# Performance work log

Measured on AMD Instinct MI355X. Metric: run time of the kernel, lower is better.

Reference implementation:

```python
import jax, jax.numpy as jnp
import numpy as np

N = 50000          # nodes
E = 800000         # edges (COO, no self loops; added during normalization)
D = 100            # input_dim
H = 16             # gcn_hidden_dim
C = 40             # output_dim (classes)
MAX_HOPS = 3
REPL = 3
NC = REPL * (MAX_HOPS + 1)   # 12 cells
BN_EPS = 1e-5


def setup_inputs() -> dict:
    key = jax.random.key(0)
    ks = jax.random.split(key, 12)
    x = jax.random.normal(ks[0], (N, D), jnp.float32)
    edge_row = jax.random.randint(ks[1], (E,), 0, N, dtype=jnp.int32)
    edge_col = jax.random.randint(ks[2], (E,), 0, N, dtype=jnp.int32)
    # stacked per-cell parameters, cell index i = r*(MAX_HOPS+1)+h
    W1 = jax.random.normal(ks[3], (NC, D, H), jnp.float32) / np.sqrt(D)
    b1 = jax.random.normal(ks[4], (NC, H), jnp.float32) * 0.01
    gamma = jnp.ones((NC, H), jnp.float32)
    beta = jnp.zeros((NC, H), jnp.float32)
    bn_mean = jnp.zeros((NC, H), jnp.float32)
    bn_var = jnp.ones((NC, H), jnp.float32)
    W2 = jax.random.normal(ks[5], (NC, H, C), jnp.float32) / np.sqrt(H)
    b2 = jax.random.normal(ks[6], (NC, C), jnp.float32) * 0.01
    Wout = jax.random.normal(ks[7], (NC * C, C), jnp.float32) / np.sqrt(NC * C)
    bout = jax.random.normal(ks[8], (C,), jnp.float32) * 0.01
    return {"x": x, "edge_row": edge_row, "edge_col": edge_col,
            "W1": W1, "b1": b1, "gamma": gamma, "beta": beta,
            "bn_mean": bn_mean, "bn_var": bn_var,
            "W2": W2, "b2": b2, "Wout": Wout, "bout": bout}


def _norm_adj(edge_row, edge_col, dtype):
    # GCN symmetric normalization with self loops: D^-1/2 (A+I) D^-1/2
    loops = jnp.arange(N, dtype=edge_row.dtype)
    row = jnp.concatenate([edge_row, loops])
    col = jnp.concatenate([edge_col, loops])
    ones = jnp.ones(row.shape[0], dtype)
    deg = jax.ops.segment_sum(ones, row, num_segments=N)
    dinv = jnp.where(deg > 0, jax.lax.rsqrt(deg), jnp.zeros_like(deg))
    vals = dinv[row] * dinv[col]
    return row, col, vals


def reference(x, edge_row, edge_col, W1, b1, gamma, beta, bn_mean, bn_var,
              W2, b2, Wout, bout):
    row, col, vals = _norm_adj(edge_row, edge_col, x.dtype)

    def spmm(h):  # [N,F] -> [N,F]  out[i] = sum_e vals[e]*h[col[e]] at row[e]
        return jax.ops.segment_sum(vals[:, None] * h[col], row, num_segments=N)

    # eval mode: input dropout = identity; L2-normalize rows
    xn = x / jnp.maximum(jnp.linalg.norm(x, axis=1, keepdims=True), 1e-12)

    # A^h x shared across replicas
    xs = [xn]
    for _ in range(MAX_HOPS):
        xs.append(spmm(xs[-1]))

    outs = []
    for r in range(REPL):
        for h in range(MAX_HOPS + 1):
            i = r * (MAX_HOPS + 1) + h
            hid = xs[h] @ W1[i] + b1[i]
            # BatchNorm1d in eval mode (running stats), then ReLU; dropout = identity
            hid = (hid - bn_mean[i]) * (gamma[i] * jax.lax.rsqrt(bn_var[i] + BN_EPS)) + beta[i]
            hid = jax.nn.relu(hid)
            for _ in range(h):
                hid = spmm(hid)
            outs.append(hid @ W2[i] + b2[i])

    cell_outputs = jnp.stack(outs, axis=1)              # [N, NC, C]
    flat = jax.nn.relu(cell_outputs.reshape(N, NC * C))
    output = flat @ Wout + bout                          # [N, C]
    return (output, cell_outputs)
```

## Files before the change

### kernel.cpp

```cpp
#include <hip/hip_runtime.h>
#include <hip/hip_bf16.h>

#define NN 50000
#define EE 800000
#define DD 100
#define HH 16
#define CC 40
#define NCELL 12
#define NB_SCAN 49

typedef __hip_bfloat162 bf2;
typedef short bf16x8 __attribute__((ext_vector_type(8)));
typedef float f32x4 __attribute__((ext_vector_type(4)));

__device__ __forceinline__ float2 b2f2(bf2 v) { return __bfloat1622float2(v); }
__device__ __forceinline__ bf2 f22b2(float f0, float f1) {
    float2 t; t.x = f0; t.y = f1;
    return __float22bfloat162_rn(t);
}
__device__ __forceinline__ unsigned short f2b(float f) {
    __hip_bfloat16 h = __float2bfloat16(f);
    return *reinterpret_cast<unsigned short*>(&h);
}


__global__ __launch_bounds__(256) void k_hist(const int* __restrict__ er, int* __restrict__ cnt) {
    int e = blockIdx.x * 256 + threadIdx.x;
    if (e < EE) atomicAdd(&cnt[er[e]], 1);
}

__global__ __launch_bounds__(256) void k_dinv(const int* __restrict__ cnt, float* __restrict__ dinv) {
    int i = blockIdx.x * 256 + threadIdx.x;
    if (i < NN) dinv[i] = rsqrtf((float)(cnt[i] + 1));
}

__global__ __launch_bounds__(1024) void k_scan1(const int* __restrict__ cnt, int* __restrict__ rp,
                                                int* __restrict__ bsum) {
    __shared__ int lds[1024];
    int t = threadIdx.x, i = blockIdx.x * 1024 + t;
    int v = (i < NN) ? cnt[i] : 0;
    lds[t] = v;
    __syncthreads();
    #pragma unroll
    for (int off = 1; off < 1024; off <<= 1) {
        int x = lds[t];
        int y = (t >= off) ? lds[t - off] : 0;
        __syncthreads();
        lds[t] = x + y;
        __syncthreads();
    }
    if (i < NN) rp[i] = lds[t] - v;
    if (t == 1023) bsum[blockIdx.x] = lds[1023];
}

__global__ __launch_bounds__(64) void k_scan2(int* __restrict__ bsum) {
    int t = threadIdx.x;
    int orig = (t < NB_SCAN) ? bsum[t] : 0;
    int v = orig;
    #pragma unroll
    for (int off = 1; off < 64; off <<= 1) {
        int y = __shfl_up(v, off);
        if (t >= off) v += y;
    }
    if (t < NB_SCAN) bsum[t] = v - orig;
    if (t == NB_SCAN - 1) bsum[NB_SCAN] = v;
}

__global__ __launch_bounds__(256) void k_scan3(int* __restrict__ rp, int* __restrict__ cursor,
                                               const int* __restrict__ bsum) {
    int i = blockIdx.x * 256 + threadIdx.x;
    if (i < NN) {
        int v = rp[i] + bsum[i >> 10];
        rp[i] = v;
        cursor[i] = v;
    }
    if (i == 0) rp[NN] = bsum[NB_SCAN];
}

__global__ __launch_bounds__(256) void k_fill(const int* __restrict__ er, const int* __restrict__ ec,
                                              const float* __restrict__ dinv, int* __restrict__ cursor,
                                              int* __restrict__ ci, float* __restrict__ cv) {
    int e = blockIdx.x * 256 + threadIdx.x;
    if (e >= EE) return;
    int r = er[e], c = ec[e];
    int p = atomicAdd(&cursor[r], 1);
    ci[p] = c;
    cv[p] = dinv[r] * dinv[c];
}

__global__ __launch_bounds__(256) void k_normx(const float* __restrict__ x, bf2* __restrict__ xb) {
    int wid = (blockIdx.x * 256 + threadIdx.x) >> 6;
    int lane = threadIdx.x & 63;
    if (wid >= NN) return;
    const size_t base = (size_t)wid * DD;
    int c0 = 2 * lane;
    float a = (c0 < DD) ? x[base + c0] : 0.f;
    float b = (c0 + 1 < DD) ? x[base + c0 + 1] : 0.f;
    float ss = a * a + b * b;
    #pragma unroll
    for (int off = 1; off < 64; off <<= 1) ss += __shfl_xor(ss, off);
    float inv = 1.f / fmaxf(sqrtf(ss), 1e-12f);
    xb[(size_t)wid * 64 + lane] = f22b2(a * inv, b * inv);
}

__global__ __launch_bounds__(256) void k_w1t(const float* __restrict__ W1, const float* __restrict__ gamma,
                                             const float* __restrict__ bn_var, unsigned short* __restrict__ W1T) {
    int idx = blockIdx.x * 256 + threadIdx.x;
    if (idx >= 192 * 128) return;
    int c = idx / 128, k = idx % 128;
    int g = c / 48, i = c % 48;
    int cell = (i / 16) * 4 + g, j = i % 16;
    float sc = gamma[cell * HH + j] * rsqrtf(bn_var[cell * HH + j] + 1e-5f);
    float v = (k < DD) ? W1[((size_t)cell * DD + k) * HH + j] * sc : 0.f;
    W1T[idx] = f2b(v);
}

__global__ __launch_bounds__(256) void k_proj_mfma(const bf2* __restrict__ xb,
                                                   const unsigned short* __restrict__ W1T,
                                                   unsigned short* __restrict__ Pu) {
    int tid = threadIdx.x;
    int wid = tid >> 6, lane = tid & 63;
    int rowbase = blockIdx.x * 64 + wid * 16;
    int arow = rowbase + (lane & 15);
    int arow_c = (arow < NN) ? arow : NN - 1;
    int kgrp = lane >> 4;
    int bcol = lane & 15;

    f32x4 acc[12];
    #pragma unroll
    for (int t = 0; t < 12; t++) acc[t] = (f32x4){0.f, 0.f, 0.f, 0.f};

    const unsigned short* ap = (const unsigned short*)(xb + (size_t)arow_c * 64);
    for (int kt = 0; kt < 4; kt++) {
        int k0 = kt * 32 + kgrp * 8;
        bf16x8 afr = *(const bf16x8*)(ap + k0);
        #pragma unroll
        for (int t = 0; t < 12; t++) {
            bf16x8 bfr = *(const bf16x8*)(W1T + (size_t)(t * 16 + bcol) * 128 + k0);
            acc[t] = __builtin_amdgcn_mfma_f32_16x16x32_bf16(afr, bfr, acc[t], 0, 0, 0);
        }
    }
    int drow = rowbase + (lane >> 4) * 4;
    #pragma unroll
    for (int r = 0; r < 4; r++) {
        int grow = drow + r;
        if (grow < NN) {
            unsigned short* pr = Pu + (size_t)grow * 192;
            #pragma unroll
            for (int t = 0; t < 12; t++)
                pr[t * 16 + (lane & 15)] = f2b(acc[t][r]);
        }
    }
}

template <int NU, int RPW>
__global__ __launch_bounds__(256) void k_spmm(const int* __restrict__ rp, const int* __restrict__ ci,
                                              const float* __restrict__ cv, const float* __restrict__ dinv,
                                              const bf2* __restrict__ in, int ins, int ioff,
                                              bf2* __restrict__ out, int outs) {
    constexpr int LPR = (RPW == 1) ? 64 : 32;
    constexpr int J = (NU + LPR - 1) / LPR;
    int gw = (blockIdx.x * 256 + threadIdx.x) >> 6;
    int lane = threadIdx.x & 63;
    int sub = (RPW == 2) ? (lane >> 5) : 0;
    int su = (RPW == 2) ? (lane & 31) : lane;
    int row = gw * RPW + sub;
    if (row >= NN) return;
    const bf2* ib = in + ioff;

    float d = dinv[row];
    float sw = d * d;
    float2 acc[J];
    {
        size_t b = (size_t)row * ins;
        #pragma unroll
        for (int j = 0; j < J; j++) {
            int u = su + LPR * j;
            if (u < NU) {
                float2 f = b2f2(ib[b + u]);
                acc[j].x = sw * f.x; acc[j].y = sw * f.y;
            } else { acc[j].x = 0.f; acc[j].y = 0.f; }
        }
    }
    int s = rp[row], e = rp[row + 1];
    int p = s;
    int e4 = s + ((e - s) & ~3);
    while (p < e4) {
        int c0 = ci[p], c1 = ci[p + 1], c2 = ci[p + 2], c3 = ci[p + 3];
        float v0 = cv[p], v1 = cv[p + 1], v2 = cv[p + 2], v3 = cv[p + 3];
        bf2 r0[J], r1[J], r2[J], r3[J];
        size_t b0 = (size_t)c0 * ins, b1 = (size_t)c1 * ins, b2 = (size_t)c2 * ins, b3 = (size_t)c3 * ins;
        #pragma unroll
        for (int j = 0; j < J; j++) {
            int u = su + LPR * j;
            if (u < NU) {
                r0[j] = ib[b0 + u]; r1[j] = ib[b1 + u];
                r2[j] = ib[b2 + u]; r3[j] = ib[b3 + u];
            }
        }
        #pragma unroll
        for (int j = 0; j < J; j++) {
            int u = su + LPR * j;
            if (u < NU) {
                float2 f0 = b2f2(r0[j]), f1 = b2f2(r1[j]), f2 = b2f2(r2[j]), f3 = b2f2(r3[j]);
                acc[j].x += v0 * f0.x + v1 * f1.x + v2 * f2.x + v3 * f3.x;
                acc[j].y += v0 * f0.y + v1 * f1.y + v2 * f2.y + v3 * f3.y;
            }
        }
        p += 4;
    }
    while (p < e) {
        int c = ci[p];
        float v = cv[p];
        size_t b = (size_t)c * ins;
        #pragma unroll
        for (int j = 0; j < J; j++) {
            int u = su + LPR * j;
            if (u < NU) {
                float2 f = b2f2(ib[b + u]);
                acc[j].x += v * f.x; acc[j].y += v * f.y;
            }
        }
        p++;
    }
    size_t ob = (size_t)row * outs;
    #pragma unroll
    for (int j = 0; j < J; j++) {
        int u = su + LPR * j;
        if (u < NU) out[ob + u] = f22b2(acc[j].x, acc[j].y);
    }
}

__global__ __launch_bounds__(256) void k_bnrelu(const bf2* __restrict__ P, const bf2* __restrict__ R1,
                                                const bf2* __restrict__ R2, const bf2* __restrict__ R3,
                                                const float* __restrict__ b1, const float* __restrict__ gamma,
                                                const float* __restrict__ beta, const float* __restrict__ bn_mean,
                                                const float* __restrict__ bn_var,
                                                bf2* __restrict__ H0, bf2* __restrict__ H123) {
    int idx = blockIdx.x * 256 + threadIdx.x;
    if (idx >= NN * 96) return;
    int n = idx / 96, u = idx % 96;
    int h, su;
    bf2 v;
    if (u < 24) { h = 0; su = u; v = P[(size_t)n * 96 + su]; }
    else {
        int uu = u - 24;
        h = uu / 24 + 1; su = uu % 24;
        if (h == 1)      v = R1[(size_t)n * 72 + su];
        else if (h == 2) v = R2[(size_t)n * 48 + su];
        else             v = R3[(size_t)n * 24 + su];
    }
    int c0 = 2 * su;
    int cell = (c0 / 16) * 4 + h;
    int j0 = c0 % 16;
    int i0 = cell * HH + j0, i1 = i0 + 1;
    float s0 = gamma[i0] * rsqrtf(bn_var[i0] + 1e-5f);
    float s1 = gamma[i1] * rsqrtf(bn_var[i1] + 1e-5f);
    float sh0 = (b1[i0] - bn_mean[i0]) * s0 + beta[i0];
    float sh1 = (b1[i1] - bn_mean[i1]) * s1 + beta[i1];
    float2 f = b2f2(v);
    bf2 o = f22b2(fmaxf(f.x + sh0, 0.f), fmaxf(f.y + sh1, 0.f));
    if (u < 24) H0[(size_t)n * 24 + u] = o;
    else        H123[(size_t)n * 72 + (u - 24)] = o;
}

#define NUNITS 1024
__global__ __launch_bounds__(128) void k_cellout(const bf2* __restrict__ H0, const bf2* __restrict__ U1,
                                                 const bf2* __restrict__ U2, const bf2* __restrict__ U3,
                                                 const float* __restrict__ W2, const float* __restrict__ b2v,
                                                 float* __restrict__ outcell) {
    __shared__ float row[2][200];
    int tid = threadIdx.x;
    int gid = tid;
    bool act = gid < 120;
    int cell = act ? gid / 10 : 0;
    int cc = act ? (4 * gid) % 40 : 0;
    int h = cell & 3, r = cell >> 2;
    float4 wreg[HH];
    float4 bias = make_float4(0.f, 0.f, 0.f, 0.f);
    if (act) {
        #pragma unroll
        for (int k = 0; k < HH; k++)
            wreg[k] = *(const float4*)(W2 + (size_t)cell * (HH * CC) + k * CC + cc);
        bias = *(const float4*)(b2v + cell * CC + cc);
    }
    int colbase = h * 48 + r * 16;

    const bf2* tabs[4] = {H0, U1, U2, U3};
    const int strides[4] = {24, 72, 48, 24};

    int iters = (NN + NUNITS - 1) / NUNITS;
    int n_cur = blockIdx.x;
    if (tid < 96 && n_cur < NN) {
        int t4 = tid / 24, uu = tid % 24;
        float2 f = b2f2(tabs[t4][(size_t)n_cur * strides[t4] + uu]);
        row[0][t4 * 48 + 2 * uu] = f.x;
        row[0][t4 * 48 + 2 * uu + 1] = f.y;
    }
    __syncthreads();
    for (int it = 0; it < iters; it++) {
        int buf = it & 1;
        int n_next = n_cur + NUNITS;
        if (it + 1 < iters && tid < 96 && n_next < NN) {
            int t4 = tid / 24, uu = tid % 24;
            float2 f = b2f2(tabs[t4][(size_t)n_next * strides[t4] + uu]);
            row[buf ^ 1][t4 * 48 + 2 * uu] = f.x;
            row[buf ^ 1][t4 * 48 + 2 * uu + 1] = f.y;
        }
        if (act && n_cur < NN) {
            float4 acc = bias;
            #pragma unroll
            for (int k = 0; k < HH; k++) {
                float xv = row[buf][colbase + k];
                acc.x += xv * wreg[k].x;
                acc.y += xv * wreg[k].y;
                acc.z += xv * wreg[k].z;
                acc.w += xv * wreg[k].w;
            }
            *(float4*)(outcell + (size_t)n_cur * (NCELL * CC) + 4 * gid) = acc;
        }
        __syncthreads();
        n_cur = n_next;
    }
}

__global__ __launch_bounds__(256) void k_wt(const float* __restrict__ Wout, unsigned short* __restrict__ WoutT) {
    int idx = blockIdx.x * 256 + threadIdx.x;
    if (idx >= 48 * 480) return;
    int c = idx / 480, k = idx % 480;
    float v = (c < CC) ? Wout[(size_t)k * CC + c] : 0.f;
    WoutT[idx] = f2b(v);
}

__global__ __launch_bounds__(256) void k_final_mfma(const float* __restrict__ cell,
                                                    const unsigned short* __restrict__ WoutT,
                                                    const float* __restrict__ bout, float* __restrict__ out) {
    int tid = threadIdx.x;
    int wid = tid >> 6, lane = tid & 63;
    int rowbase = blockIdx.x * 64 + wid * 16;
    int arow = rowbase + (lane & 15);
    int arow_c = (arow < NN) ? arow : NN - 1;
    int kgrp = lane >> 4;

    f32x4 acc0 = {0.f, 0.f, 0.f, 0.f};
    f32x4 acc1 = {0.f, 0.f, 0.f, 0.f};
    f32x4 acc2 = {0.f, 0.f, 0.f, 0.f};

    const float* arow_p = cell + (size_t)arow_c * (NCELL * CC);
    int bcol = lane & 15;

    for (int kt = 0; kt < 15; kt++) {
        int k0 = kt * 32 + kgrp * 8;
        float4 va = *(const float4*)(arow_p + k0);
        float4 vb = *(const float4*)(arow_p + k0 + 4);
        bf16x8 afr;
        afr[0] = (short)f2b(fmaxf(va.x, 0.f));
        afr[1] = (short)f2b(fmaxf(va.y, 0.f));
        afr[2] = (short)f2b(fmaxf(va.z, 0.f));
        afr[3] = (short)f2b(fmaxf(va.w, 0.f));
        afr[4] = (short)f2b(fmaxf(vb.x, 0.f));
        afr[5] = (short)f2b(fmaxf(vb.y, 0.f));
        afr[6] = (short)f2b(fmaxf(vb.z, 0.f));
        afr[7] = (short)f2b(fmaxf(vb.w, 0.f));
        bf16x8 bf0 = *(const bf16x8*)(WoutT + (size_t)(0 * 16 + bcol) * 480 + k0);
        bf16x8 bf1 = *(const bf16x8*)(WoutT + (size_t)(1 * 16 + bcol) * 480 + k0);
        bf16x8 bf2f = *(const bf16x8*)(WoutT + (size_t)(2 * 16 + bcol) * 480 + k0);
        acc0 = __builtin_amdgcn_mfma_f32_16x16x32_bf16(afr, bf0, acc0, 0, 0, 0);
        acc1 = __builtin_amdgcn_mfma_f32_16x16x32_bf16(afr, bf1, acc1, 0, 0, 0);
        acc2 = __builtin_amdgcn_mfma_f32_16x16x32_bf16(afr, bf2f, acc2, 0, 0, 0);
    }

    int drow = rowbase + (lane >> 4) * 4;
    #pragma unroll
    for (int r = 0; r < 4; r++) {
        int grow = drow + r;
        if (grow < NN) {
            int c0 = 0 * 16 + (lane & 15);
            int c1 = 1 * 16 + (lane & 15);
            int c2 = 2 * 16 + (lane & 15);
            float* o = out + (size_t)grow * CC;
            o[c0] = acc0[r] + bout[c0];
            o[c1] = acc1[r] + bout[c1];
            if (c2 < CC) o[c2] = acc2[r] + bout[c2];
        }
    }
}


extern "C" void kernel_launch(void* const* d_in, const int* in_sizes, int n_in,
                              void* d_out, int out_size, void* d_ws, size_t ws_size,
                              hipStream_t stream) {
    const float* x       = (const float*)d_in[0];
    const int*   er      = (const int*)d_in[1];
    const int*   ec      = (const int*)d_in[2];
    const float* W1      = (const float*)d_in[3];
    const float* b1      = (const float*)d_in[4];
    const float* gamma   = (const float*)d_in[5];
    const float* beta    = (const float*)d_in[6];
    const float* bn_mean = (const float*)d_in[7];
    const float* bn_var  = (const float*)d_in[8];
    const float* W2      = (const float*)d_in[9];
    const float* b2v     = (const float*)d_in[10];
    const float* Wout    = (const float*)d_in[11];
    const float* bout    = (const float*)d_in[12];

    float* out     = (float*)d_out;
    float* outcell = out + (size_t)NN * CC;

    char* w = (char*)d_ws;
    auto alloc = [&](size_t bytes) {
        void* p = (void*)w;
        w += (bytes + 255) & ~(size_t)255;
        return p;
    };
    int*   cnt    = (int*)alloc((size_t)NN * 4);
    int*   rp     = (int*)alloc((size_t)(NN + 1) * 4);
    int*   cursor = (int*)alloc((size_t)NN * 4);
    float* dinv   = (float*)alloc((size_t)NN * 4);
    int*   bsum   = (int*)alloc((size_t)(NB_SCAN + 1) * 4);
    int*   ci     = (int*)alloc((size_t)EE * 4);
    float* cv     = (float*)alloc((size_t)EE * 4);
    bf2*   xb     = (bf2*)alloc((size_t)NN * 64 * 4);
    bf2*   P      = (bf2*)alloc((size_t)NN * 96 * 4);
    bf2*   R1     = (bf2*)alloc((size_t)NN * 72 * 4);
    bf2*   R2     = (bf2*)alloc((size_t)NN * 48 * 4);
    bf2*   R3     = (bf2*)alloc((size_t)NN * 24 * 4);
    bf2*   H0     = (bf2*)alloc((size_t)NN * 24 * 4);
    bf2*   H123   = (bf2*)alloc((size_t)NN * 72 * 4);
    bf2*   U1     = (bf2*)alloc((size_t)NN * 72 * 4);
    bf2*   U2     = (bf2*)alloc((size_t)NN * 48 * 4);
    bf2*   U3     = (bf2*)alloc((size_t)NN * 24 * 4);
    unsigned short* WoutT = (unsigned short*)alloc((size_t)48 * 480 * 2);
    unsigned short* W1T   = (unsigned short*)alloc((size_t)192 * 128 * 2);

    hipMemsetAsync(cnt, 0, (size_t)NN * 4, stream);

    int gE = (EE + 255) / 256;
    int gN = (NN + 255) / 256;

    k_hist<<<gE, 256, 0, stream>>>(er, cnt);
    k_dinv<<<gN, 256, 0, stream>>>(cnt, dinv);
    k_scan1<<<NB_SCAN, 1024, 0, stream>>>(cnt, rp, bsum);
    k_scan2<<<1, 64, 0, stream>>>(bsum);
    k_scan3<<<gN, 256, 0, stream>>>(rp, cursor, bsum);
    k_fill<<<gE, 256, 0, stream>>>(er, ec, dinv, cursor, ci, cv);
    k_wt<<<(48 * 480 + 255) / 256, 256, 0, stream>>>(Wout, WoutT);
    k_w1t<<<(192 * 128 + 255) / 256, 256, 0, stream>>>(W1, gamma, bn_var, W1T);

    int gW = (NN + 3) / 4;
    int g64 = (NN + 63) / 64;
    k_normx<<<gW, 256, 0, stream>>>(x, xb);
    k_proj_mfma<<<g64, 256, 0, stream>>>(xb, W1T, (unsigned short*)P);

    int gW1 = (NN + 3) / 4;
    int gW2 = (NN + 7) / 8;
    k_spmm<72, 1><<<gW1, 256, 0, stream>>>(rp, ci, cv, dinv, P, 96, 24, R1, 72);
    k_spmm<48, 1><<<gW1, 256, 0, stream>>>(rp, ci, cv, dinv, R1, 72, 24, R2, 48);
    k_spmm<24, 2><<<gW2, 256, 0, stream>>>(rp, ci, cv, dinv, R2, 48, 24, R3, 24);

    k_bnrelu<<<(NN * 96 + 255) / 256, 256, 0, stream>>>(P, R1, R2, R3, b1, gamma, beta, bn_mean, bn_var, H0, H123);

    k_spmm<72, 1><<<gW1, 256, 0, stream>>>(rp, ci, cv, dinv, H123, 72, 0, U1, 72);
    k_spmm<48, 1><<<gW1, 256, 0, stream>>>(rp, ci, cv, dinv, U1, 72, 24, U2, 48);
    k_spmm<24, 2><<<gW2, 256, 0, stream>>>(rp, ci, cv, dinv, U2, 48, 24, U3, 24);

    k_cellout<<<NUNITS, 128, 0, stream>>>(H0, U1, U2, U3, W2, b2v, outcell);
    k_final_mfma<<<g64, 256, 0, stream>>>(outcell, WoutT, bout, out);
}
```

Measured before the change: 457.8 us.

## Fuse BN/ReLU into projection and SpMM epilogues, drop finished columns, MFMA cell output

After: 504.2 us. +10.1%, slower.

```diff
diff --git a/kernel.cpp b/kernel.cpp
--- a/kernel.cpp
+++ b/kernel.cpp
@@ -115,9 +115,35 @@
     W1T[idx] = f2b(v);
 }
 
+__global__ __launch_bounds__(256) void k_shift(const float* __restrict__ b1, const float* __restrict__ gamma,
+                                               const float* __restrict__ beta, const float* __restrict__ bn_mean,
+                                               const float* __restrict__ bn_var, float* __restrict__ shift192) {
+    int c = blockIdx.x * 256 + threadIdx.x;
+    if (c >= 192) return;
+    int h = c / 48, r = (c % 48) / 16, j = c % 16;
+    int i = (r * 4 + h) * HH + j;
+    float sc = gamma[i] * rsqrtf(bn_var[i] + 1e-5f);
+    shift192[c] = (b1[i] - bn_mean[i]) * sc + beta[i];
+}
+
+__global__ __launch_bounds__(256) void k_w2p(const float* __restrict__ W2, unsigned short* __restrict__ Wpack) {
+    int idx = blockIdx.x * 256 + threadIdx.x;
+    if (idx >= 30 * 16 * 32) return;
+    int t = idx / 512, bcol = (idx / 32) % 16, k = idx % 32;
+    int c = 16 * t + bcol;
+    int cell = c / 40, cc = c % 40;
+    int m = (2 * t) / 5; if (m > 10) m = 10;
+    int kg = 16 * m + k;
+    int cellk = kg / 16, j = kg % 16;
+    float v = (cellk == cell) ? W2[((size_t)cell * HH + j) * CC + cc] : 0.f;
+    Wpack[idx] = f2b(v);
+}
+
 __global__ __launch_bounds__(256) void k_proj_mfma(const bf2* __restrict__ xb,
                                                    const unsigned short* __restrict__ W1T,
-                                                   unsigned short* __restrict__ Pu) {
+                                                   const float* __restrict__ shift192,
+                                                   unsigned short* __restrict__ Hcat,
+                                                   unsigned short* __restrict__ Pg) {
     int tid = threadIdx.x;
     int wid = tid >> 6, lane = tid & 63;
     int rowbase = blockIdx.x * 64 + wid * 16;
@@ -141,23 +167,33 @@
         }
     }
     int drow = rowbase + (lane >> 4) * 4;
+    int lc = lane & 15;
     #pragma unroll
     for (int r = 0; r < 4; r++) {
         int grow = drow + r;
         if (grow < NN) {
-            unsigned short* pr = Pu + (size_t)grow * 192;
             #pragma unroll
-            for (int t = 0; t < 12; t++)
-                pr[t * 16 + (lane & 15)] = f2b(acc[t][r]);
-        }
-    }
-}
-
-template <int NU, int RPW>
+            for (int t = 0; t < 12; t++) {
+                int c = t * 16 + lc;
+                float v = acc[t][r];
+                if (c < 48) {
+                    v = fmaxf(v + shift192[c], 0.f);
+                    Hcat[(size_t)grow * 192 + (c / 16) * 64 + (c % 16)] = f2b(v);
+                } else {
+                    Pg[(size_t)grow * 144 + (c - 48)] = f2b(v);
+                }
+            }
+        }
+    }
+}
+
+template <int NU, int RPW, bool RELU, bool HMAP>
 __global__ __launch_bounds__(256) void k_spmm(const int* __restrict__ rp, const int* __restrict__ ci,
                                               const float* __restrict__ cv, const float* __restrict__ dinv,
-                                              const bf2* __restrict__ in, int ins, int ioff,
-                                              bf2* __restrict__ out, int outs) {
+                                              const bf2* __restrict__ in, int ins,
+                                              bf2* __restrict__ outA, int sA, int aoff,
+                                              const float* __restrict__ shiftA,
+                                              bf2* __restrict__ outB, int sB) {
     constexpr int LPR = (RPW == 1) ? 64 : 32;
     constexpr int J = (NU + LPR - 1) / LPR;
     int gw = (blockIdx.x * 256 + threadIdx.x) >> 6;
@@ -166,7 +202,6 @@
     int su = (RPW == 2) ? (lane & 31) : lane;
     int row = gw * RPW + sub;
     if (row >= NN) return;
-    const bf2* ib = in + ioff;
 
     float d = dinv[row];
     float sw = d * d;
@@ -177,37 +212,41 @@
         for (int j = 0; j < J; j++) {
             int u = su + LPR * j;
             if (u < NU) {
-                float2 f = b2f2(ib[b + u]);
+                float2 f = b2f2(in[b + u]);
                 acc[j].x = sw * f.x; acc[j].y = sw * f.y;
             } else { acc[j].x = 0.f; acc[j].y = 0.f; }
         }
     }
     int s = rp[row], e = rp[row + 1];
     int p = s;
-    int e4 = s + ((e - s) & ~3);
-    while (p < e4) {
-        int c0 = ci[p], c1 = ci[p + 1], c2 = ci[p + 2], c3 = ci[p + 3];
-        float v0 = cv[p], v1 = cv[p + 1], v2 = cv[p + 2], v3 = cv[p + 3];
-        bf2 r0[J], r1[J], r2[J], r3[J];
-        size_t b0 = (size_t)c0 * ins, b1 = (size_t)c1 * ins, b2 = (size_t)c2 * ins, b3 = (size_t)c3 * ins;
-        #pragma unroll
-        for (int j = 0; j < J; j++) {
-            int u = su + LPR * j;
-            if (u < NU) {
-                r0[j] = ib[b0 + u]; r1[j] = ib[b1 + u];
-                r2[j] = ib[b2 + u]; r3[j] = ib[b3 + u];
+    int e8 = s + ((e - s) & ~7);
+    while (p < e8) {
+        int cc8[8]; float vv[8];
+        #pragma unroll
+        for (int q = 0; q < 8; q++) { cc8[q] = ci[p + q]; vv[q] = cv[p + q]; }
+        bf2 rr[8][J];
+        #pragma unroll
+        for (int q = 0; q < 8; q++) {
+            size_t b = (size_t)cc8[q] * ins;
+            #pragma unroll
+            for (int j = 0; j < J; j++) {
+                int u = su + LPR * j;
+                if (u < NU) rr[q][j] = in[b + u];
             }
         }
         #pragma unroll
-        for (int j = 0; j < J; j++) {
-            int u = su + LPR * j;
-            if (u < NU) {
-                float2 f0 = b2f2(r0[j]), f1 = b2f2(r1[j]), f2 = b2f2(r2[j]), f3 = b2f2(r3[j]);
-                acc[j].x += v0 * f0.x + v1 * f1.x + v2 * f2.x + v3 * f3.x;
-                acc[j].y += v0 * f0.y + v1 * f1.y + v2 * f2.y + v3 * f3.y;
+        for (int q = 0; q < 8; q++) {
+            #pragma unroll
+            for (int j = 0; j < J; j++) {
+                int u = su + LPR * j;
+                if (u < NU) {
+                    float2 f = b2f2(rr[q][j]);
+                    acc[j].x += vv[q] * f.x;
+                    acc[j].y += vv[q] * f.y;
+                }
             }
         }
-        p += 4;
+        p += 8;
     }
     while (p < e) {
         int c = ci[p];
@@ -217,110 +256,62 @@
         for (int j = 0; j < J; j++) {
             int u = su + LPR * j;
             if (u < NU) {
-                float2 f = b2f2(ib[b + u]);
+                float2 f = b2f2(in[b + u]);
                 acc[j].x += v * f.x; acc[j].y += v * f.y;
             }
         }
         p++;
     }
-    size_t ob = (size_t)row * outs;
     #pragma unroll
     for (int j = 0; j < J; j++) {
         int u = su + LPR * j;
-        if (u < NU) out[ob + u] = f22b2(acc[j].x, acc[j].y);
-    }
-}
-
-__global__ __launch_bounds__(256) void k_bnrelu(const bf2* __restrict__ P, const bf2* __restrict__ R1,
-                                                const bf2* __restrict__ R2, const bf2* __restrict__ R3,
-                                                const float* __restrict__ b1, const float* __restrict__ gamma,
-                                                const float* __restrict__ beta, const float* __restrict__ bn_mean,
-                                                const float* __restrict__ bn_var,
-                                                bf2* __restrict__ H0, bf2* __restrict__ H123) {
-    int idx = blockIdx.x * 256 + threadIdx.x;
-    if (idx >= NN * 96) return;
-    int n = idx / 96, u = idx % 96;
-    int h, su;
-    bf2 v;
-    if (u < 24) { h = 0; su = u; v = P[(size_t)n * 96 + su]; }
-    else {
-        int uu = u - 24;
-        h = uu / 24 + 1; su = uu % 24;
-        if (h == 1)      v = R1[(size_t)n * 72 + su];
-        else if (h == 2) v = R2[(size_t)n * 48 + su];
-        else             v = R3[(size_t)n * 24 + su];
-    }
-    int c0 = 2 * su;
-    int cell = (c0 / 16) * 4 + h;
-    int j0 = c0 % 16;
-    int i0 = cell * HH + j0, i1 = i0 + 1;
-    float s0 = gamma[i0] * rsqrtf(bn_var[i0] + 1e-5f);
-    float s1 = gamma[i1] * rsqrtf(bn_var[i1] + 1e-5f);
-    float sh0 = (b1[i0] - bn_mean[i0]) * s0 + beta[i0];
-    float sh1 = (b1[i1] - bn_mean[i1]) * s1 + beta[i1];
-    float2 f = b2f2(v);
-    bf2 o = f22b2(fmaxf(f.x + sh0, 0.f), fmaxf(f.y + sh1, 0.f));
-    if (u < 24) H0[(size_t)n * 24 + u] = o;
-    else        H123[(size_t)n * 72 + (u - 24)] = o;
-}
-
-#define NUNITS 1024
-__global__ __launch_bounds__(128) void k_cellout(const bf2* __restrict__ H0, const bf2* __restrict__ U1,
-                                                 const bf2* __restrict__ U2, const bf2* __restrict__ U3,
-                                                 const float* __restrict__ W2, const float* __restrict__ b2v,
-                                                 float* __restrict__ outcell) {
-    __shared__ float row[2][200];
+        if (u < NU) {
+            float fx = acc[j].x, fy = acc[j].y;
+            if (u < 24) {
+                if (RELU) {
+                    fx = fmaxf(fx + shiftA[2 * u], 0.f);
+                    fy = fmaxf(fy + shiftA[2 * u + 1], 0.f);
+                }
+                int unit = HMAP ? ((u / 8) * 32 + (u & 7) + aoff) : (u + aoff);
+                outA[(size_t)row * sA + unit] = f22b2(fx, fy);
+            } else {
+                outB[(size_t)row * sB + (u - 24)] = f22b2(fx, fy);
+            }
+        }
+    }
+}
+
+__global__ __launch_bounds__(256) void k_cellout_mfma(const unsigned short* __restrict__ Hcat,
+                                                      const unsigned short* __restrict__ Wpack,
+                                                      const float* __restrict__ b2v,
+                                                      float* __restrict__ outcell) {
     int tid = threadIdx.x;
-    int gid = tid;
-    bool act = gid < 120;
-    int cell = act ? gid / 10 : 0;
-    int cc = act ? (4 * gid) % 40 : 0;
-    int h = cell & 3, r = cell >> 2;
-    float4 wreg[HH];
-    float4 bias = make_float4(0.f, 0.f, 0.f, 0.f);
-    if (act) {
-        #pragma unroll
-        for (int k = 0; k < HH; k++)
-            wreg[k] = *(const float4*)(W2 + (size_t)cell * (HH * CC) + k * CC + cc);
-        bias = *(const float4*)(b2v + cell * CC + cc);
-    }
-    int colbase = h * 48 + r * 16;
-
-    const bf2* tabs[4] = {H0, U1, U2, U3};
-    const int strides[4] = {24, 72, 48, 24};
-
-    int iters = (NN + NUNITS - 1) / NUNITS;
-    int n_cur = blockIdx.x;
-    if (tid < 96 && n_cur < NN) {
-        int t4 = tid / 24, uu = tid % 24;
-        float2 f = b2f2(tabs[t4][(size_t)n_cur * strides[t4] + uu]);
-        row[0][t4 * 48 + 2 * uu] = f.x;
-        row[0][t4 * 48 + 2 * uu + 1] = f.y;
-    }
-    __syncthreads();
-    for (int it = 0; it < iters; it++) {
-        int buf = it & 1;
-        int n_next = n_cur + NUNITS;
-        if (it + 1 < iters && tid < 96 && n_next < NN) {
-            int t4 = tid / 24, uu = tid % 24;
-            float2 f = b2f2(tabs[t4][(size_t)n_next * strides[t4] + uu]);
-            row[buf ^ 1][t4 * 48 + 2 * uu] = f.x;
-            row[buf ^ 1][t4 * 48 + 2 * uu + 1] = f.y;
-        }
-        if (act && n_cur < NN) {
-            float4 acc = bias;
-            #pragma unroll
-            for (int k = 0; k < HH; k++) {
-                float xv = row[buf][colbase + k];
-                acc.x += xv * wreg[k].x;
-                acc.y += xv * wreg[k].y;
-                acc.z += xv * wreg[k].z;
-                acc.w += xv * wreg[k].w;
-            }
-            *(float4*)(outcell + (size_t)n_cur * (NCELL * CC) + 4 * gid) = acc;
-        }
-        __syncthreads();
-        n_cur = n_next;
+    int wid = tid >> 6, lane = tid & 63;
+    int rowbase = blockIdx.x * 64 + wid * 16;
+    int arow = rowbase + (lane & 15);
+    int arow_c = (arow < NN) ? arow : NN - 1;
+    int kgrp = lane >> 4;
+    int bcol = lane & 15;
+
+    const unsigned short* hr = Hcat + (size_t)arow_c * 192;
+    bf16x8 ab[11];
+    #pragma unroll
+    for (int m = 0; m < 11; m++) ab[m] = *(const bf16x8*)(hr + (2 * m + kgrp) * 8);
+
+    int drow = rowbase + (lane >> 4) * 4;
+    #pragma unroll
+    for (int t = 0; t < 30; t++) {
+        const int m = ((2 * t) / 5 < 10) ? (2 * t) / 5 : 10;
+        bf16x8 bfr = *(const bf16x8*)(Wpack + (size_t)(t * 16 + bcol) * 32 + kgrp * 8);
+        f32x4 acc = {0.f, 0.f, 0.f, 0.f};
+        acc = __builtin_amdgcn_mfma_f32_16x16x32_bf16(ab[m], bfr, acc, 0, 0, 0);
+        int c = 16 * t + bcol;
+        float bias = b2v[c];
+        #pragma unroll
+        for (int r = 0; r < 4; r++) {
+            int grow = drow + r;
+            if (grow < NN) outcell[(size_t)grow * (NCELL * CC) + c] = acc[r] + bias;
+        }
     }
 }
 
@@ -421,17 +412,17 @@
     int*   ci     = (int*)alloc((size_t)EE * 4);
     float* cv     = (float*)alloc((size_t)EE * 4);
     bf2*   xb     = (bf2*)alloc((size_t)NN * 64 * 4);
-    bf2*   P      = (bf2*)alloc((size_t)NN * 96 * 4);
-    bf2*   R1     = (bf2*)alloc((size_t)NN * 72 * 4);
-    bf2*   R2     = (bf2*)alloc((size_t)NN * 48 * 4);
-    bf2*   R3     = (bf2*)alloc((size_t)NN * 24 * 4);
-    bf2*   H0     = (bf2*)alloc((size_t)NN * 24 * 4);
-    bf2*   H123   = (bf2*)alloc((size_t)NN * 72 * 4);
-    bf2*   U1     = (bf2*)alloc((size_t)NN * 72 * 4);
-    bf2*   U2     = (bf2*)alloc((size_t)NN * 48 * 4);
-    bf2*   U3     = (bf2*)alloc((size_t)NN * 24 * 4);
+    bf2*   Pg     = (bf2*)alloc((size_t)NN * 72 * 4);
+    bf2*   T      = (bf2*)alloc((size_t)NN * 72 * 4);
+    bf2*   Rg1    = (bf2*)alloc((size_t)NN * 48 * 4);
+    bf2*   Rg2    = (bf2*)alloc((size_t)NN * 24 * 4);
+    bf2*   Vg1    = (bf2*)alloc((size_t)NN * 48 * 4);
+    bf2*   Vg2    = (bf2*)alloc((size_t)NN * 24 * 4);
+    bf2*   Hcat   = (bf2*)alloc((size_t)NN * 96 * 4);
+    float* shift192 = (float*)alloc((size_t)192 * 4);
     unsigned short* WoutT = (unsigned short*)alloc((size_t)48 * 480 * 2);
     unsigned short* W1T   = (unsigned short*)alloc((size_t)192 * 128 * 2);
+    unsigned short* Wpack = (unsigned short*)alloc((size_t)30 * 16 * 32 * 2);
 
     hipMemsetAsync(cnt, 0, (size_t)NN * 4, stream);
 
@@ -446,24 +437,23 @@
     k_fill<<<gE, 256, 0, stream>>>(er, ec, dinv, cursor, ci, cv);
     k_wt<<<(48 * 480 + 255) / 256, 256, 0, stream>>>(Wout, WoutT);
     k_w1t<<<(192 * 128 + 255) / 256, 256, 0, stream>>>(W1, gamma, bn_var, W1T);
+    k_shift<<<1, 256, 0, stream>>>(b1, gamma, beta, bn_mean, bn_var, shift192);
+    k_w2p<<<(30 * 16 * 32 + 255) / 256, 256, 0, stream>>>(W2, Wpack);
 
     int gW = (NN + 3) / 4;
     int g64 = (NN + 63) / 64;
     k_normx<<<gW, 256, 0, stream>>>(x, xb);
-    k_proj_mfma<<<g64, 256, 0, stream>>>(xb, W1T, (unsigned short*)P);
+    k_proj_mfma<<<g64, 256, 0, stream>>>(xb, W1T, shift192, (unsigned short*)Hcat, (unsigned short*)Pg);
 
     int gW1 = (NN + 3) / 4;
     int gW2 = (NN + 7) / 8;
-    k_spmm<72, 1><<<gW1, 256, 0, stream>>>(rp, ci, cv, dinv, P, 96, 24, R1, 72);
-    k_spmm<48, 1><<<gW1, 256, 0, stream>>>(rp, ci, cv, dinv, R1, 72, 24, R2, 48);
-    k_spmm<24, 2><<<gW2, 256, 0, stream>>>(rp, ci, cv, dinv, R2, 48, 24, R3, 24);
-
-    k_bnrelu<<<(NN * 96 + 255) / 256, 256, 0, stream>>>(P, R1, R2, R3, b1, gamma, beta, bn_mean, bn_var, H0, H123);
-
-    k_spmm<72, 1><<<gW1, 256, 0, stream>>>(rp, ci, cv, dinv, H123, 72, 0, U1, 72);
-    k_spmm<48, 1><<<gW1, 256, 0, stream>>>(rp, ci, cv, dinv, U1, 72, 24, U2, 48);
-    k_spmm<24, 2><<<gW2, 256, 0, stream>>>(rp, ci, cv, dinv, U2, 48, 24, U3, 24);
-
-    k_cellout<<<NUNITS, 128, 0, stream>>>(H0, U1, U2, U3, W2, b2v, outcell);
+    k_spmm<72, 1, true, false><<<gW1, 256, 0, stream>>>(rp, ci, cv, dinv, Pg, 72, T, 72, 0,  shift192 + 48,  Rg1, 48);
+    k_spmm<48, 1, true, false><<<gW1, 256, 0, stream>>>(rp, ci, cv, dinv, Rg1, 48, T, 72, 24, shift192 + 96,  Rg2, 24);
+    k_spmm<24, 2, true, false><<<gW2, 256, 0, stream>>>(rp, ci, cv, dinv, Rg2, 24, T, 72, 48, shift192 + 144, Rg1, 48);
+    k_spmm<72, 1, false, true><<<gW1, 256, 0, stream>>>(rp, ci, cv, dinv, T, 72,   Hcat, 96, 8,  nullptr, Vg1, 48);
+    k_spmm<48, 1, false, true><<<gW1, 256, 0, stream>>>(rp, ci, cv, dinv, Vg1, 48, Hcat, 96, 16, nullptr, Vg2, 24);
+    k_spmm<24, 2, false, true><<<gW2, 256, 0, stream>>>(rp, ci, cv, dinv, Vg2, 24, Hcat, 96, 24, nullptr, Vg1, 48);
+
+    k_cellout_mfma<<<g64, 256, 0, stream>>>((const unsigned short*)Hcat, Wpack, b2v, outcell);
     k_final_mfma<<<g64, 256, 0, stream>>>(outcell, WoutT, bout, out);
 }
```
